# Optimization experiments

Measured on AMD Instinct MI355X. Metric: run time of the kernel, lower is better.

Reference implementation:

```python
import jax, jax.numpy as jnp
import numpy as np

HEADS = 8
CPH = 32


def _rel_pos_indices(h, w):
    # same construction as the torch buffer, done statically in numpy
    coords = np.stack(np.meshgrid(np.arange(h), np.arange(w), indexing='ij')).reshape(2, -1)  # [2, N]
    rel = coords[:, :, None] - coords[:, None, :]  # [2, N, N]
    idx = (rel[0] + h - 1) * (2 * w - 1) + (rel[1] + w - 1)  # [N, N]
    return jnp.asarray(idx, dtype=jnp.int32)


def setup_inputs() -> dict:
    key = jax.random.key(0)
    ks = jax.random.split(key, 6)
    B, C, H, W = 2, 256, 48, 48
    emb = HEADS * CPH  # 256
    x = jax.random.normal(ks[0], (B, C, H, W), dtype=jnp.float32)
    # GDN params (kept positive so sqrt is well-defined)
    gdn_beta = jnp.ones((C,), dtype=jnp.float32)
    gdn_gamma = 0.1 * jnp.eye(C, dtype=jnp.float32) + 0.001 * jax.random.uniform(ks[1], (C, C), dtype=jnp.float32)
    w_qkv = 0.02 * jax.random.normal(ks[2], (3 * emb, C), dtype=jnp.float32)
    w_out = 0.02 * jax.random.normal(ks[3], (C, emb), dtype=jnp.float32)
    b_out = jnp.zeros((C,), dtype=jnp.float32)
    table_size = (2 * H - 1) * (2 * W - 1)
    rel_bias_table = 0.02 * jax.random.normal(ks[4], (table_size, HEADS), dtype=jnp.float32)
    return {"x": x, "gdn_beta": gdn_beta, "gdn_gamma": gdn_gamma,
            "w_qkv": w_qkv, "w_out": w_out, "b_out": b_out,
            "rel_bias_table": rel_bias_table}


def reference(x, gdn_beta, gdn_gamma, w_qkv, w_out, b_out, rel_bias_table):
    B, C, H, W = x.shape
    N = H * W
    emb = HEADS * CPH
    scale = CPH ** (-0.5)

    # GDN: y = x / sqrt(beta + gamma * x^2)  (1x1 conv over channels of x^2)
    norm = jnp.einsum('bchw,dc->bdhw', x * x, gdn_gamma) + gdn_beta[None, :, None, None]
    xn = x / jnp.sqrt(norm)

    # flatten spatial, channels last: [B, N, C]
    t = xn.reshape(B, C, N).transpose(0, 2, 1)

    # qkv projection (no bias)
    qkv = (t @ w_qkv.T).reshape(B, N, 3, HEADS, CPH).transpose(2, 0, 3, 1, 4)  # [3, B, h, N, d]
    q, k, v = qkv[0], qkv[1], qkv[2]

    attn = jnp.einsum('bhnd,bhmd->bhnm', q, k) * scale  # [B, h, N, N]

    # gathered relative position bias: [h, N, N]
    idx = _rel_pos_indices(H, W)  # [N, N], static ints
    bias = rel_bias_table[idx.reshape(-1)].reshape(N, N, HEADS).transpose(2, 0, 1)
    attn = jax.nn.softmax(attn + bias[None], axis=-1)

    # NOTE: faithful to the original quirk — reshape (B, h, N, d) directly
    # to (B, N, C) with NO head/seq transpose, exactly like the torch code.
    res = jnp.einsum('bhnm,bhmd->bhnd', attn, v).reshape(B, N, emb)

    out = res @ w_out.T + b_out  # [B, N, C]
    return out.transpose(0, 2, 1).reshape(B, C, H, W)
```

## Files before the change

### kernel.cpp

```cpp
#include <hip/hip_runtime.h>
#include <cstdint>
#include <cstddef>

typedef __attribute__((ext_vector_type(8))) short short8;
typedef __attribute__((ext_vector_type(4))) float floatx4;
typedef __attribute__((ext_vector_type(4))) unsigned short ushort4v;

#define NB 2
#define NPIX 2304
#define TBL 9025
#define TBLP 9032
#define L2E 1.4426950408889634f
#define QSCALE 0.17677669529663689f

__device__ __forceinline__ float b2f(unsigned short u) {
  union { unsigned int i; float f; } v; v.i = ((unsigned int)u) << 16; return v.f;
}
__device__ __forceinline__ unsigned short f2b(float f) {
  union { float f; unsigned int i; } v; v.f = f;
  return (unsigned short)((v.i + 0x7fffu + ((v.i >> 16) & 1u)) >> 16);
}
__device__ __forceinline__ unsigned int cvtpk(float lo, float hi) {
  unsigned int r;
  asm("v_cvt_pk_bf16_f32 %0, %1, %2" : "=v"(r) : "v"(lo), "v"(hi));
  return r;
}

__global__ __launch_bounds__(256) void prep_k(
    const float* __restrict__ gamma, const float* __restrict__ wqkv,
    const float* __restrict__ wout, const float* __restrict__ table,
    const float* __restrict__ x,
    unsigned short* __restrict__ gb, unsigned short* __restrict__ qb,
    unsigned short* __restrict__ wb, unsigned short* __restrict__ tb,
    unsigned short* __restrict__ xsq)
{
  __shared__ unsigned short Ls[64][66];
  const int bx = blockIdx.x;
  const int tid = threadIdx.x;
  if (bx < 768) {
    int i = bx * 256 + tid;
    if (i < 65536)  gb[i] = f2b(gamma[i]);
    qb[i] = f2b(wqkv[i]);
    if (i < 65536)  wb[i] = f2b(wout[i]);
    if (i < TBL * 8) {
      int e = i >> 3, h = i & 7;
      tb[(size_t)h * TBLP + e] = f2b(table[i] * L2E);
    }
    return;
  }
  const int t = bx - 768;
  const int b = t / 144, r = t % 144;
  const int c0 = (r / 36) * 64, n0 = (r % 36) * 64;
  {
    const int ci = tid >> 2, ng = (tid & 3) * 16;
    const float* xr = &x[((size_t)(b * 256 + c0 + ci)) * NPIX + n0 + ng];
    unsigned int* dst = (unsigned int*)&Ls[ci][ng];
    #pragma unroll
    for (int j = 0; j < 4; ++j) {
      float4 v = *(const float4*)(xr + j * 4);
      dst[j * 2]     = cvtpk(v.x * v.x, v.y * v.y);
      dst[j * 2 + 1] = cvtpk(v.z * v.z, v.w * v.w);
    }
  }
  __syncthreads();
  {
    const int nr = tid >> 2, cc = (tid & 3) * 16;
    unsigned short* orow = &xsq[((size_t)(b * NPIX) + n0 + nr) * 256 + c0 + cc];
    unsigned short tmp[16];
    #pragma unroll
    for (int j = 0; j < 16; ++j) tmp[j] = Ls[cc + j][nr];
    *(short8*)&orow[0] = *(short8*)&tmp[0];
    *(short8*)&orow[8] = *(short8*)&tmp[8];
  }
}

template<int MODE>
__global__ __launch_bounds__(256) void gemm_k(
    const unsigned short* __restrict__ A,
    const unsigned short* __restrict__ Bw,
    const float* __restrict__ vec,
    const float* __restrict__ X,
    unsigned short* __restrict__ o0,
    unsigned short* __restrict__ o1,
    unsigned short* __restrict__ o2,
    float* __restrict__ of)
{
  const int n0 = blockIdx.x * 64;
  const int m0 = blockIdx.y * 64;
  const int b  = blockIdx.z;
  const int tid = threadIdx.x;
  const int wave = tid >> 6, lane = tid & 63;
  const int wm = wave >> 1, wn = wave & 1;
  const int lm = lane & 15, quad = lane >> 4;

  const unsigned short* pa = &A[(size_t)(m0 + wm * 32 + lm) * 256 + quad * 8];
  const unsigned short* pb = &Bw[((size_t)b * NPIX + n0 + wn * 32 + lm) * 256 + quad * 8];

  floatx4 acc[2][2] = {};
  #pragma unroll
  for (int k0 = 0; k0 < 256; k0 += 32) {
    short8 af0 = *(const short8*)(pa + k0);
    short8 af1 = *(const short8*)(pa + 16 * 256 + k0);
    short8 bf0 = *(const short8*)(pb + k0);
    short8 bf1 = *(const short8*)(pb + 16 * 256 + k0);
    acc[0][0] = __builtin_amdgcn_mfma_f32_16x16x32_bf16(af0, bf0, acc[0][0], 0, 0, 0);
    acc[0][1] = __builtin_amdgcn_mfma_f32_16x16x32_bf16(af0, bf1, acc[0][1], 0, 0, 0);
    acc[1][0] = __builtin_amdgcn_mfma_f32_16x16x32_bf16(af1, bf0, acc[1][0], 0, 0, 0);
    acc[1][1] = __builtin_amdgcn_mfma_f32_16x16x32_bf16(af1, bf1, acc[1][1], 0, 0, 0);
  }

  #pragma unroll
  for (int tm = 0; tm < 2; ++tm) {
    const int rbase = m0 + wm * 32 + tm * 16 + quad * 4;
    #pragma unroll
    for (int tn = 0; tn < 2; ++tn) {
      const int col = n0 + wn * 32 + tn * 16 + lm;
      floatx4 a4 = acc[tm][tn];
      if (MODE == 0) {
        float xn[4];
        #pragma unroll
        for (int r = 0; r < 4; ++r) {
          int d = rbase + r;
          float xv = X[((size_t)(b * 256 + d)) * NPIX + col];
          xn[r] = xv * rsqrtf(vec[d] + a4[r]);
        }
        uint2 pk = { cvtpk(xn[0], xn[1]), cvtpk(xn[2], xn[3]) };
        *(uint2*)&o0[((size_t)(b * NPIX + col)) * 256 + rbase] = pk;
      } else if (MODE == 1) {
        const int part = rbase >> 8, h = (rbase >> 5) & 7, dd = rbase & 31;
        if (part == 2) {
          #pragma unroll
          for (int r = 0; r < 4; ++r)
            o2[(((size_t)(b * 8 + h)) * 32 + dd + r) * NPIX + col] = f2b(a4[r]);
        } else {
          unsigned short* dst = part == 0 ? o0 : o1;
          const float sc = (part == 0) ? (QSCALE * L2E) : 1.0f;
          uint2 pk = { cvtpk(a4[0] * sc, a4[1] * sc), cvtpk(a4[2] * sc, a4[3] * sc) };
          *(uint2*)&dst[(((size_t)(b * 8 + h)) * NPIX + col) * 32 + dd] = pk;
        }
      } else {
        #pragma unroll
        for (int r = 0; r < 4; ++r) {
          int c = rbase + r;
          of[((size_t)(b * 256 + c)) * NPIX + col] = a4[r] + vec[c];
        }
      }
    }
  }
}

__global__ __launch_bounds__(256) void attn_k(
    const unsigned short* __restrict__ qg, const unsigned short* __restrict__ kg,
    const unsigned short* __restrict__ vt, const unsigned short* __restrict__ tabt,
    unsigned short* __restrict__ ob)
{
  __shared__ __align__(16) unsigned short tab[TBLP];
  __shared__ __align__(16) unsigned short Pl[4][16][72];

  const int tid = threadIdx.x;
  const int w = tid >> 6, lane = tid & 63;
  const int lm = lane & 15, quad = lane >> 4;
  const int q0 = blockIdx.x * 64;
  const int bh = blockIdx.y;
  const size_t base = (size_t)bh * NPIX * 32;

  {
    const unsigned short* src = tabt + (size_t)(bh & 7) * TBLP;
    for (int e = tid * 8; e < TBLP; e += 2048)
      *(short8*)&tab[e] = *(const short8*)&src[e];
  }
  __syncthreads();

  const int q = q0 + w * 16 + lm;
  const short8 qfrag = *(const short8*)&qg[base + (size_t)q * 32 + quad * 8];

  const int hi = (q * 43691) >> 21;
  const int rb = (hi + 47) * 95 + (q - hi * 48) + 47;

  float lsum = 0.f;
  floatx4 o[2] = {};

  for (int t = 0; t < 36; ++t) {
    const int j0 = t * 64;
    floatx4 s4[4];
    #pragma unroll
    for (int kt = 0; kt < 4; ++kt) {
      short8 kf = *(const short8*)&kg[base + (size_t)(j0 + kt * 16 + lm) * 32 + quad * 8];
      floatx4 z = {};
      s4[kt] = __builtin_amdgcn_mfma_f32_16x16x32_bf16(kf, qfrag, z, 0, 0, 0);
    }
    #pragma unroll
    for (int kt = 0; kt < 4; ++kt) {
      const int kk = j0 + kt * 16 + quad * 4;
      const int hj = (kk * 43691) >> 21;
      const int bbase = rb - kk - hj * 47;
      float pv[4];
      #pragma unroll
      for (int r = 0; r < 4; ++r) {
        float p = exp2f(s4[kt][r] + b2f(tab[bbase - r]));
        lsum += p;
        pv[r] = p;
      }
      uint2 pk = { cvtpk(pv[0], pv[1]), cvtpk(pv[2], pv[3]) };
      *(uint2*)&Pl[w][lm][kt * 16 + quad * 4] = pk;
    }
    __asm__ volatile("s_waitcnt lgkmcnt(0)" ::: "memory");
    #pragma unroll
    for (int c = 0; c < 2; ++c) {
      short8 pf = *(const short8*)&Pl[w][lm][c * 32 + quad * 8];
      #pragma unroll
      for (int dt = 0; dt < 2; ++dt) {
        short8 vf = *(const short8*)&vt[base + (size_t)(dt * 16 + lm) * NPIX + j0 + c * 32 + quad * 8];
        o[dt] = __builtin_amdgcn_mfma_f32_16x16x32_bf16(vf, pf, o[dt], 0, 0, 0);
      }
    }
  }

  lsum += __shfl_xor(lsum, 16, 64);
  lsum += __shfl_xor(lsum, 32, 64);
  const float inv = 1.f / lsum;

  #pragma unroll
  for (int dt = 0; dt < 2; ++dt) {
    uint2 pk = { cvtpk(o[dt][0] * inv, o[dt][1] * inv),
                 cvtpk(o[dt][2] * inv, o[dt][3] * inv) };
    *(uint2*)&ob[base + (size_t)q * 32 + dt * 16 + quad * 4] = pk;
  }
}

extern "C" void kernel_launch(void* const* d_in, const int* in_sizes, int n_in,
                              void* d_out, int out_size, void* d_ws, size_t ws_size,
                              hipStream_t stream) {
  const float* x     = (const float*)d_in[0];
  const float* beta  = (const float*)d_in[1];
  const float* gamma = (const float*)d_in[2];
  const float* wqkv  = (const float*)d_in[3];
  const float* wout  = (const float*)d_in[4];
  const float* bout  = (const float*)d_in[5];
  const float* table = (const float*)d_in[6];
  float* out = (float*)d_out;

  unsigned short* ws = (unsigned short*)d_ws;
  const size_t NE = (size_t)NB * NPIX * 256;
  unsigned short* xn_t  = ws;
  unsigned short* qbuf  = ws + NE;
  unsigned short* kbuf  = ws + 2 * NE;
  unsigned short* vtbuf = ws + 3 * NE;
  unsigned short* obuf  = ws + 4 * NE;
  unsigned short* gam_b = obuf;
  unsigned short* qkv_b = obuf + 65536;
  unsigned short* out_b = ws + 5 * NE;
  unsigned short* tab_t = ws + 5 * NE + 65536;
  unsigned short* xsq   = qbuf;

  prep_k<<<1056, 256, 0, stream>>>(gamma, wqkv, wout, table, x,
                                   gam_b, qkv_b, out_b, tab_t, xsq);
  gemm_k<0><<<dim3(36, 4, 2), 256, 0, stream>>>(gam_b, xsq, beta, x,
                                                xn_t, nullptr, nullptr, nullptr);
  gemm_k<1><<<dim3(36, 12, 2), 256, 0, stream>>>(qkv_b, xn_t, nullptr, nullptr,
                                                 qbuf, kbuf, vtbuf, nullptr);
  attn_k<<<dim3(36, 16), 256, 0, stream>>>(qbuf, kbuf, vtbuf, tab_t, obuf);
  gemm_k<2><<<dim3(36, 4, 2), 256, 0, stream>>>(out_b, obuf, bout, nullptr,
                                                nullptr, nullptr, nullptr, out);
}
```

Measured before the change: 183.2 us.

## Split attention keys across two blocks and reduce partials in a new kernel

The attention kernel now splits the key range in two (split-K), doubling the grid from 576 to 1152 blocks so more of the GPU's CUs are busy. Each block writes fp32 partial outputs and row sums, and a new reduce kernel combines them and normalises. The bias table is no longer staged in LDS; it is read straight from global memory. The row sum is now computed with an extra MFMA against a vector of ones instead of scalar adds. These changes add an extra launch, fp32 partial traffic, and uncached-in-LDS gathers from the table.

After: 190.8 us. 4.2% more time.

```diff
diff --git a/kernel.cpp b/kernel.cpp
--- a/kernel.cpp
+++ b/kernel.cpp
@@ -4,7 +4,6 @@
 
 typedef __attribute__((ext_vector_type(8))) short short8;
 typedef __attribute__((ext_vector_type(4))) float floatx4;
-typedef __attribute__((ext_vector_type(4))) unsigned short ushort4v;
 
 #define NB 2
 #define NPIX 2304
@@ -12,6 +11,8 @@
 #define TBLP 9032
 #define L2E 1.4426950408889634f
 #define QSCALE 0.17677669529663689f
+#define SPLIT 2
+#define TILES_PER_SPLIT 18
 
 __device__ __forceinline__ float b2f(unsigned short u) {
   union { unsigned int i; float f; } v; v.i = ((unsigned int)u) << 16; return v.f;
@@ -152,24 +153,18 @@
 __global__ __launch_bounds__(256) void attn_k(
     const unsigned short* __restrict__ qg, const unsigned short* __restrict__ kg,
     const unsigned short* __restrict__ vt, const unsigned short* __restrict__ tabt,
-    unsigned short* __restrict__ ob)
-{
-  __shared__ __align__(16) unsigned short tab[TBLP];
+    float* __restrict__ po, float* __restrict__ pl)
+{
   __shared__ __align__(16) unsigned short Pl[4][16][72];
 
   const int tid = threadIdx.x;
   const int w = tid >> 6, lane = tid & 63;
   const int lm = lane & 15, quad = lane >> 4;
-  const int q0 = blockIdx.x * 64;
-  const int bh = blockIdx.y;
+  const int bh = blockIdx.x;
+  const int q0 = blockIdx.y * 64;
+  const int s  = blockIdx.z;
   const size_t base = (size_t)bh * NPIX * 32;
-
-  {
-    const unsigned short* src = tabt + (size_t)(bh & 7) * TBLP;
-    for (int e = tid * 8; e < TBLP; e += 2048)
-      *(short8*)&tab[e] = *(const short8*)&src[e];
-  }
-  __syncthreads();
+  const unsigned short* __restrict__ tabg = tabt + (size_t)(bh & 7) * TBLP;
 
   const int q = q0 + w * 16 + lm;
   const short8 qfrag = *(const short8*)&qg[base + (size_t)q * 32 + quad * 8];
@@ -177,11 +172,14 @@
   const int hi = (q * 43691) >> 21;
   const int rb = (hi + 47) * 95 + (q - hi * 48) + 47;
 
-  float lsum = 0.f;
   floatx4 o[2] = {};
-
-  for (int t = 0; t < 36; ++t) {
-    const int j0 = t * 64;
+  floatx4 ol = {};
+  short8 ones;
+  #pragma unroll
+  for (int j = 0; j < 8; ++j) ones[j] = (short)0x3F80;
+
+  for (int tt = 0; tt < TILES_PER_SPLIT; ++tt) {
+    const int j0 = (s * TILES_PER_SPLIT + tt) * 64;
     floatx4 s4[4];
     #pragma unroll
     for (int kt = 0; kt < 4; ++kt) {
@@ -193,14 +191,11 @@
     for (int kt = 0; kt < 4; ++kt) {
       const int kk = j0 + kt * 16 + quad * 4;
       const int hj = (kk * 43691) >> 21;
-      const int bbase = rb - kk - hj * 47;
+      const int bb = rb - kk - hj * 47;
       float pv[4];
       #pragma unroll
-      for (int r = 0; r < 4; ++r) {
-        float p = exp2f(s4[kt][r] + b2f(tab[bbase - r]));
-        lsum += p;
-        pv[r] = p;
-      }
+      for (int r = 0; r < 4; ++r)
+        pv[r] = exp2f(s4[kt][r] + b2f(tabg[bb - r]));
       uint2 pk = { cvtpk(pv[0], pv[1]), cvtpk(pv[2], pv[3]) };
       *(uint2*)&Pl[w][lm][kt * 16 + quad * 4] = pk;
     }
@@ -208,6 +203,7 @@
     #pragma unroll
     for (int c = 0; c < 2; ++c) {
       short8 pf = *(const short8*)&Pl[w][lm][c * 32 + quad * 8];
+      ol = __builtin_amdgcn_mfma_f32_16x16x32_bf16(ones, pf, ol, 0, 0, 0);
       #pragma unroll
       for (int dt = 0; dt < 2; ++dt) {
         short8 vf = *(const short8*)&vt[base + (size_t)(dt * 16 + lm) * NPIX + j0 + c * 32 + quad * 8];
@@ -216,16 +212,29 @@
     }
   }
 
-  lsum += __shfl_xor(lsum, 16, 64);
-  lsum += __shfl_xor(lsum, 32, 64);
-  const float inv = 1.f / lsum;
-
-  #pragma unroll
-  for (int dt = 0; dt < 2; ++dt) {
-    uint2 pk = { cvtpk(o[dt][0] * inv, o[dt][1] * inv),
-                 cvtpk(o[dt][2] * inv, o[dt][3] * inv) };
-    *(uint2*)&ob[base + (size_t)q * 32 + dt * 16 + quad * 4] = pk;
-  }
+  const size_t pbase = ((size_t)(s * 16 + bh) * NPIX + q) * 32;
+  *(floatx4*)&po[pbase + quad * 4]      = o[0];
+  *(floatx4*)&po[pbase + 16 + quad * 4] = o[1];
+  if (quad == 0) pl[(size_t)(s * 16 + bh) * NPIX + q] = ol[0];
+}
+
+__global__ __launch_bounds__(256) void reduce_k(
+    const float* __restrict__ po, const float* __restrict__ pl,
+    unsigned short* __restrict__ ob)
+{
+  const int tid = threadIdx.x;
+  const int bh = blockIdx.y;
+  const int q = blockIdx.x * 32 + (tid >> 3);
+  const int d4 = (tid & 7) * 4;
+  const size_t st = (size_t)16 * NPIX * 32;
+  const size_t i0 = ((size_t)bh * NPIX + q) * 32 + d4;
+  floatx4 a = *(const floatx4*)&po[i0];
+  floatx4 b = *(const floatx4*)&po[i0 + st];
+  a += b;
+  const size_t li = (size_t)bh * NPIX + q;
+  const float inv = 1.f / (pl[li] + pl[li + (size_t)16 * NPIX]);
+  uint2 pk = { cvtpk(a[0] * inv, a[1] * inv), cvtpk(a[2] * inv, a[3] * inv) };
+  *(uint2*)&ob[((size_t)bh * NPIX + q) * 32 + d4] = pk;
 }
 
 extern "C" void kernel_launch(void* const* d_in, const int* in_sizes, int n_in,
@@ -251,6 +260,8 @@
   unsigned short* qkv_b = obuf + 65536;
   unsigned short* out_b = ws + 5 * NE;
   unsigned short* tab_t = ws + 5 * NE + 65536;
+  float* po = (float*)(ws + 5 * NE + 65536 + 8 * TBLP);
+  float* pl = po + (size_t)SPLIT * 16 * NPIX * 32;
   unsigned short* xsq   = qbuf;
 
   prep_k<<<1056, 256, 0, stream>>>(gamma, wqkv, wout, table, x,
@@ -259,7 +270,8 @@
                                                 xn_t, nullptr, nullptr, nullptr);
   gemm_k<1><<<dim3(36, 12, 2), 256, 0, stream>>>(qkv_b, xn_t, nullptr, nullptr,
                                                  qbuf, kbuf, vtbuf, nullptr);
-  attn_k<<<dim3(36, 16), 256, 0, stream>>>(qbuf, kbuf, vtbuf, tab_t, obuf);
+  attn_k<<<dim3(16, 36, SPLIT), 256, 0, stream>>>(qbuf, kbuf, vtbuf, tab_t, po, pl);
+  reduce_k<<<dim3(72, 16), 256, 0, stream>>>(po, pl, obuf);
   gemm_k<2><<<dim3(36, 4, 2), 256, 0, stream>>>(out_b, obuf, bout, nullptr,
                                                 nullptr, nullptr, nullptr, out);
 }
```

## Prefetch next K tile and bias from global, drop LDS bias table

Applied to the files above, without the earlier changes.

The attention kernel no longer copies the per-head relative-bias table (about 18 KB) into shared memory. It reads bias values straight from global memory and software-prefetches the next tile's K fragments and bias values into registers while the current tile is processed. V loads are issued at the start of each tile, and the grid is transposed so that consecutive blocks share a (batch, head) and its K/V data in cache. This is meant to remove the table-copy prologue and barrier, cut LDS use so more blocks fit per CU, and hide global load latency. The cost is higher register pressure and scattered 2-byte global gathers for the bias.

Measured after the change: 199.5 us. 8.9% more time.

```diff
diff --git a/kernel.cpp b/kernel.cpp
--- a/kernel.cpp
+++ b/kernel.cpp
@@ -4,7 +4,6 @@
 
 typedef __attribute__((ext_vector_type(8))) short short8;
 typedef __attribute__((ext_vector_type(4))) float floatx4;
-typedef __attribute__((ext_vector_type(4))) unsigned short ushort4v;
 
 #define NB 2
 #define NPIX 2304
@@ -12,6 +11,7 @@
 #define TBLP 9032
 #define L2E 1.4426950408889634f
 #define QSCALE 0.17677669529663689f
+#define NTILES 36
 
 __device__ __forceinline__ float b2f(unsigned short u) {
   union { unsigned int i; float f; } v; v.i = ((unsigned int)u) << 16; return v.f;
@@ -154,22 +154,15 @@
     const unsigned short* __restrict__ vt, const unsigned short* __restrict__ tabt,
     unsigned short* __restrict__ ob)
 {
-  __shared__ __align__(16) unsigned short tab[TBLP];
   __shared__ __align__(16) unsigned short Pl[4][16][72];
 
   const int tid = threadIdx.x;
   const int w = tid >> 6, lane = tid & 63;
   const int lm = lane & 15, quad = lane >> 4;
-  const int q0 = blockIdx.x * 64;
-  const int bh = blockIdx.y;
+  const int bh = blockIdx.x;
+  const int q0 = blockIdx.y * 64;
   const size_t base = (size_t)bh * NPIX * 32;
-
-  {
-    const unsigned short* src = tabt + (size_t)(bh & 7) * TBLP;
-    for (int e = tid * 8; e < TBLP; e += 2048)
-      *(short8*)&tab[e] = *(const short8*)&src[e];
-  }
-  __syncthreads();
+  const unsigned short* __restrict__ tabg = tabt + (size_t)(bh & 7) * TBLP;
 
   const int q = q0 + w * 16 + lm;
   const short8 qfrag = *(const short8*)&qg[base + (size_t)q * 32 + quad * 8];
@@ -180,24 +173,61 @@
   float lsum = 0.f;
   floatx4 o[2] = {};
 
-  for (int t = 0; t < 36; ++t) {
-    const int j0 = t * 64;
+  short8 kf[4];
+  unsigned short br[16];
+  {
+    #pragma unroll
+    for (int kt = 0; kt < 4; ++kt)
+      kf[kt] = *(const short8*)&kg[base + (size_t)(kt * 16 + lm) * 32 + quad * 8];
+    #pragma unroll
+    for (int kt = 0; kt < 4; ++kt) {
+      const int kk = kt * 16 + quad * 4;
+      const int hj = (kk * 43691) >> 21;
+      const int bb = rb - kk - hj * 47;
+      #pragma unroll
+      for (int r = 0; r < 4; ++r) br[kt * 4 + r] = tabg[bb - r];
+    }
+  }
+
+  for (int tt = 0; tt < NTILES; ++tt) {
+    const int j0 = tt * 64;
+    const int tn = (tt + 1 < NTILES) ? tt + 1 : tt;
+    const int j0n = tn * 64;
+
+    short8 vf[2][2];
+    #pragma unroll
+    for (int c = 0; c < 2; ++c)
+      #pragma unroll
+      for (int dt = 0; dt < 2; ++dt)
+        vf[c][dt] = *(const short8*)&vt[base + (size_t)(dt * 16 + lm) * NPIX + j0 + c * 32 + quad * 8];
+
     floatx4 s4[4];
     #pragma unroll
     for (int kt = 0; kt < 4; ++kt) {
-      short8 kf = *(const short8*)&kg[base + (size_t)(j0 + kt * 16 + lm) * 32 + quad * 8];
       floatx4 z = {};
-      s4[kt] = __builtin_amdgcn_mfma_f32_16x16x32_bf16(kf, qfrag, z, 0, 0, 0);
-    }
-    #pragma unroll
-    for (int kt = 0; kt < 4; ++kt) {
-      const int kk = j0 + kt * 16 + quad * 4;
+      s4[kt] = __builtin_amdgcn_mfma_f32_16x16x32_bf16(kf[kt], qfrag, z, 0, 0, 0);
+    }
+
+    short8 kfn[4];
+    unsigned short brn[16];
+    #pragma unroll
+    for (int kt = 0; kt < 4; ++kt)
+      kfn[kt] = *(const short8*)&kg[base + (size_t)(j0n + kt * 16 + lm) * 32 + quad * 8];
+    #pragma unroll
+    for (int kt = 0; kt < 4; ++kt) {
+      const int kk = j0n + kt * 16 + quad * 4;
       const int hj = (kk * 43691) >> 21;
-      const int bbase = rb - kk - hj * 47;
+      const int bb = rb - kk - hj * 47;
+      #pragma unroll
+      for (int r = 0; r < 4; ++r) brn[kt * 4 + r] = tabg[bb - r];
+    }
+
+    #pragma unroll
+    for (int kt = 0; kt < 4; ++kt) {
       float pv[4];
       #pragma unroll
       for (int r = 0; r < 4; ++r) {
-        float p = exp2f(s4[kt][r] + b2f(tab[bbase - r]));
+        float p = exp2f(s4[kt][r] + b2f(br[kt * 4 + r]));
         lsum += p;
         pv[r] = p;
       }
@@ -205,15 +235,19 @@
       *(uint2*)&Pl[w][lm][kt * 16 + quad * 4] = pk;
     }
     __asm__ volatile("s_waitcnt lgkmcnt(0)" ::: "memory");
+
     #pragma unroll
     for (int c = 0; c < 2; ++c) {
       short8 pf = *(const short8*)&Pl[w][lm][c * 32 + quad * 8];
       #pragma unroll
-      for (int dt = 0; dt < 2; ++dt) {
-        short8 vf = *(const short8*)&vt[base + (size_t)(dt * 16 + lm) * NPIX + j0 + c * 32 + quad * 8];
-        o[dt] = __builtin_amdgcn_mfma_f32_16x16x32_bf16(vf, pf, o[dt], 0, 0, 0);
-      }
-    }
+      for (int dt = 0; dt < 2; ++dt)
+        o[dt] = __builtin_amdgcn_mfma_f32_16x16x32_bf16(vf[c][dt], pf, o[dt], 0, 0, 0);
+    }
+
+    #pragma unroll
+    for (int kt = 0; kt < 4; ++kt) kf[kt] = kfn[kt];
+    #pragma unroll
+    for (int i = 0; i < 16; ++i) br[i] = brn[i];
   }
 
   lsum += __shfl_xor(lsum, 16, 64);
@@ -259,7 +293,7 @@
                                                 xn_t, nullptr, nullptr, nullptr);
   gemm_k<1><<<dim3(36, 12, 2), 256, 0, stream>>>(qkv_b, xn_t, nullptr, nullptr,
                                                  qbuf, kbuf, vtbuf, nullptr);
-  attn_k<<<dim3(36, 16), 256, 0, stream>>>(qbuf, kbuf, vtbuf, tab_t, obuf);
+  attn_k<<<dim3(16, 36), 256, 0, stream>>>(qbuf, kbuf, vtbuf, tab_t, obuf);
   gemm_k<2><<<dim3(36, 4, 2), 256, 0, stream>>>(out_b, obuf, bout, nullptr,
                                                 nullptr, nullptr, nullptr, out);
 }
```
